# Kernel optimization log

Measured on AMD Instinct MI355X. Metric: run time of the kernel, lower is better.

## Reference

```python
import jax, jax.numpy as jnp
import numpy as np

N_SEG = 128      # number of ragged segments (boundaries has N_SEG+1 entries)
SEG_LEN = 128    # tokens per segment (regular boundaries)
D_IN = 1024      # input_size
H = 512          # hidden per direction; output_size = 2*H = 1024


def _run_dir(xs, W_ih, W_hh, b):
    """xs: [L, B, D] -> hidden states [L, B, H] for one direction.
    torch LSTM gate order: i, f, g, o."""
    xp = jnp.einsum('lbd,gd->lbg', xs, W_ih) + b  # precompute input projections [L,B,4H]
    B = xs.shape[1]
    Hh = W_hh.shape[1]

    def step(carry, gx):
        h, c = carry
        g = gx + h @ W_hh.T
        i, f, gg, o = jnp.split(g, 4, axis=-1)
        c = jax.nn.sigmoid(f) * c + jax.nn.sigmoid(i) * jnp.tanh(gg)
        h = jax.nn.sigmoid(o) * jnp.tanh(c)
        return (h, c), h

    z = jnp.zeros((B, Hh), xs.dtype)
    _, hs = jax.lax.scan(step, (z, z), xp)
    return hs


def _bilstm(x, W_ih_f, W_hh_f, b_f, W_ih_b, W_hh_b, b_b):
    hf = _run_dir(x, W_ih_f, W_hh_f, b_f)
    hb = _run_dir(x[::-1], W_ih_b, W_hh_b, b_b)[::-1]
    return jnp.concatenate([hf, hb], axis=-1)  # [L, B, 2H], fwd then bwd as in torch


def setup_inputs() -> dict:
    key = jax.random.key(0)
    ks = jax.random.split(key, 7)
    T = N_SEG * SEG_LEN
    s = 1.0 / np.sqrt(H)  # torch LSTM init scale
    u = lambda k, shape: jax.random.uniform(k, shape, jnp.float32, -s, s)
    return {
        'all_embs': jax.random.normal(ks[0], (T, D_IN), jnp.float32),
        'boundaries': jnp.arange(N_SEG + 1, dtype=jnp.int32) * SEG_LEN,
        'W_ih_f': u(ks[1], (4 * H, D_IN)),
        'W_hh_f': u(ks[2], (4 * H, H)),
        'b_f': u(ks[3], (4 * H,)),  # b_ih + b_hh folded together
        'W_ih_b': u(ks[4], (4 * H, D_IN)),
        'W_hh_b': u(ks[5], (4 * H, H)),
        'b_b': u(ks[6], (4 * H,)),
    }


def reference(all_embs, boundaries, W_ih_f, W_hh_f, b_f, W_ih_b, W_hh_b, b_b):
    n_seg = boundaries.shape[0] - 1
    T, D = all_embs.shape
    L = T // n_seg
    # regular boundaries: batch the per-segment LSTM calls into one scan
    x = all_embs.reshape(n_seg, L, D).transpose(1, 0, 2)  # [L, n_seg, D]
    y = _bilstm(x, W_ih_f, W_hh_f, b_f, W_ih_b, W_hh_b, b_b)  # [L, n_seg, 2H]
    out = y.transpose(1, 0, 2).reshape(T, 2 * H)
    # summarize=False: new boundaries equal old boundaries
    return (out, boundaries)
```

## Files before the change

kernel.cpp:

```cpp
#include <hip/hip_runtime.h>


typedef __attribute__((ext_vector_type(8))) short bf16x8;
typedef __attribute__((ext_vector_type(4))) float f32x4;

__device__ __forceinline__ unsigned short f2bf(float f) {
  unsigned int x = __builtin_bit_cast(unsigned int, f);
  x += 0x7fffu + ((x >> 16) & 1u);
  return (unsigned short)(x >> 16);
}
__device__ __forceinline__ float bf2f(unsigned short u) {
  unsigned int x = ((unsigned int)u) << 16;
  return __builtin_bit_cast(float, x);
}
__device__ __forceinline__ float sigm(float x) { return 1.f / (1.f + __expf(-x)); }
__device__ __forceinline__ float tanhfast(float x) {
  float e = __expf(2.f * x);
  return 1.f - 2.f / (e + 1.f);
}

__device__ __forceinline__ void gl_lds16(const void* g, void* l) {
  __builtin_amdgcn_global_load_lds((const __attribute__((address_space(1))) unsigned int*)g,
                                   (__attribute__((address_space(3))) unsigned int*)l, 16, 0, 0);
}
__device__ __forceinline__ void gl_lds16_llc(const void* g, void* l) {
  __builtin_amdgcn_global_load_lds((const __attribute__((address_space(1))) unsigned int*)g,
                                   (__attribute__((address_space(3))) unsigned int*)l, 16, 0, 17);
}

__global__ __launch_bounds__(256) void cast_x(const float* __restrict__ X,
                                              unsigned short* __restrict__ Xb) {
  const int i = blockIdx.x * 256 + threadIdx.x;
  const float4 v = ((const float4*)X)[i];
  uint2 o;
  o.x = (unsigned int)f2bf(v.x) | ((unsigned int)f2bf(v.y) << 16);
  o.y = (unsigned int)f2bf(v.z) | ((unsigned int)f2bf(v.w) << 16);
  ((uint2*)Xb)[i] = o;
}

__global__ __launch_bounds__(256) void pack_w(const float* __restrict__ Wif,
                                              const float* __restrict__ bf_,
                                              const float* __restrict__ Wib,
                                              const float* __restrict__ bb_,
                                              unsigned short* __restrict__ Wc,
                                              float* __restrict__ biasp) {
  const int pr = blockIdx.x;
  const int d = pr >> 11, r = pr & 2047;
  const float* src = (d ? Wib : Wif) + (size_t)r * 1024;
  const int t = threadIdx.x;
  const float4 v = ((const float4*)src)[t];
  uint2 o;
  o.x = (unsigned int)f2bf(v.x) | ((unsigned int)f2bf(v.y) << 16);
  o.y = (unsigned int)f2bf(v.z) | ((unsigned int)f2bf(v.w) << 16);
  ((uint2*)(Wc + (size_t)pr * 1024))[t] = o;
  if (t == 0) biasp[pr] = (d ? bb_ : bf_)[r];
}

__global__ __launch_bounds__(256) void gemm_xp(const unsigned short* __restrict__ A,
                                               const unsigned short* __restrict__ B,
                                               const float* __restrict__ bias,
                                               unsigned short* __restrict__ C) {
  __shared__ unsigned short SMEM[16384];
  unsigned short* As = SMEM;
  unsigned short* Bs = SMEM + 8192;
  const int tid = threadIdx.x;
  const int lane = tid & 63;
  const int wid = tid >> 6;
  const int wm = wid >> 1, wn = wid & 1;
  const long brow = (long)blockIdx.x * 128;
  const long bcol = (long)blockIdx.y * 128;

  f32x4 acc[4][4];
  const f32x4 z = {0.f, 0.f, 0.f, 0.f};
#pragma unroll
  for (int i = 0; i < 4; ++i)
#pragma unroll
    for (int j = 0; j < 4; ++j) acc[i][j] = z;

  int srow[4], scol[4];
#pragma unroll
  for (int j = 0; j < 4; ++j) {
    const int o = (j * 256 + tid) * 16;
    srow[j] = o >> 7;
    scol[j] = (o & 127) ^ ((srow[j] & 7) << 4);
  }

  for (int ks = 0; ks < 16; ++ks) {
    const int kb0 = ks * 128;
#pragma unroll
    for (int j = 0; j < 4; ++j) {
      const int o = (j * 256 + tid) * 16;
      gl_lds16((const char*)A + (brow + srow[j]) * 2048 + kb0 + scol[j], (char*)As + o);
      gl_lds16((const char*)B + (bcol + srow[j]) * 2048 + kb0 + scol[j], (char*)Bs + o);
    }
    __syncthreads();
    bf16x8 av[4][2], bv[4][2];
#pragma unroll
    for (int f = 0; f < 4; ++f) {
      const int ra = wm * 64 + f * 16 + (lane & 15);
      const int rb = wn * 64 + f * 16 + (lane & 15);
      const int swa = (ra & 7) << 4, swb = (rb & 7) << 4;
#pragma unroll
      for (int kk = 0; kk < 2; ++kk) {
        const int kby = kk * 64 + (lane >> 4) * 16;
        av[f][kk] = *(const bf16x8*)((const char*)As + ra * 128 + (kby ^ swa));
        bv[f][kk] = *(const bf16x8*)((const char*)Bs + rb * 128 + (kby ^ swb));
      }
    }
#pragma unroll
    for (int kk = 0; kk < 2; ++kk)
#pragma unroll
      for (int fm = 0; fm < 4; ++fm)
#pragma unroll
        for (int fn = 0; fn < 4; ++fn)
          acc[fm][fn] =
              __builtin_amdgcn_mfma_f32_16x16x32_bf16(av[fm][kk], bv[fn][kk], acc[fm][fn], 0, 0, 0);
    __syncthreads();
  }
  const int crow0 = wm * 64 + (lane >> 4) * 4;
  const int ccol0 = wn * 64 + (lane & 15);
#pragma unroll
  for (int fm = 0; fm < 4; ++fm) {
#pragma unroll
    for (int fn = 0; fn < 4; ++fn) {
      const int col = ccol0 + fn * 16;
      const float bsv = bias[bcol + col];
#pragma unroll
      for (int r = 0; r < 4; ++r)
        SMEM[(crow0 + fm * 16 + r) * 128 + col] = f2bf(acc[fm][fn][r] + bsv);
    }
  }
  __syncthreads();
#pragma unroll
  for (int j = 0; j < 8; ++j) {
    const int id = j * 256 + tid;
    const int row = id >> 4;
    const int c = id & 15;
    *(float4*)(C + (brow + row) * 4096 + bcol + c * 8) = *(const float4*)(SMEM + row * 128 + c * 8);
  }
}

__global__ __launch_bounds__(256, 1) void lstm_persist(
    const unsigned short* __restrict__ XPb, const float* __restrict__ Whf,
    const float* __restrict__ Whb, unsigned short* __restrict__ hb0,
    unsigned short* __restrict__ hb1, float* __restrict__ out,
    unsigned int* __restrict__ ctr) {
  __shared__ unsigned short A_s[8192];
  __shared__ unsigned short Hrep[16][32];

  const int tid = threadIdx.x;
  const int bid = blockIdx.x;
  const int ut = bid >> 4;
  const int grp = bid & 15;
  const int dir = grp >> 3;
  const int cs = grp & 7;
  const int lane = tid & 63;
  const int w = tid >> 6;
  const int p = lane & 15;
  const int kq8 = lane >> 4;
  const int hi = p >> 3;
  const int u_l = w * 8 + (p & 7);
  const int u_g = ut * 32 + u_l;
  unsigned int* const myctr = ctr + grp * 32;

  bf16x8 wreg[2][16];
  {
    const float* Wh = dir ? Whb : Whf;
#pragma unroll
    for (int f = 0; f < 2; ++f) {
      const int g = f * 2 + hi;
      const float* wrow = Wh + (size_t)(g * 512 + u_g) * 512 + kq8 * 8;
#pragma unroll
      for (int kk = 0; kk < 16; ++kk) {
        const float4 v0 = *(const float4*)(wrow + kk * 32);
        const float4 v1 = *(const float4*)(wrow + kk * 32 + 4);
        bf16x8 t;
        t[0] = (short)f2bf(v0.x); t[1] = (short)f2bf(v0.y);
        t[2] = (short)f2bf(v0.z); t[3] = (short)f2bf(v0.w);
        t[4] = (short)f2bf(v1.x); t[5] = (short)f2bf(v1.y);
        t[6] = (short)f2bf(v1.z); t[7] = (short)f2bf(v1.w);
        wreg[f][kk] = t;
      }
    }
  }

  float c_reg[2] = {0.f, 0.f};
  const size_t tileoff = (size_t)grp * 16384;
  const int cl0 = kq8 * 4 + 2 * hi;

  unsigned short xpr[2][4];
  {
    const int tcol0 = dir ? 127 : 0;
#pragma unroll
    for (int j = 0; j < 2; ++j) {
      const int seg = cs * 16 + cl0 + j;
      const size_t tok = (size_t)seg * 128 + tcol0;
      const unsigned short* xp = XPb + tok * 4096 + dir * 2048 + u_g;
#pragma unroll
      for (int g = 0; g < 4; ++g) xpr[j][g] = xp[g * 512];
    }
  }

  float phv[2];
  size_t pofs[2] = {0, 0};

  for (int tau = 0; tau < 128; ++tau) {
    const unsigned short* hc = (tau & 1) ? hb1 : hb0;
    unsigned short* hn = (tau & 1) ? hb0 : hb1;
    const int tcol = dir ? (127 - tau) : tau;

    {
      const char* srcb = (const char*)hc + tileoff;
      char* dstb = (char*)A_s;
#pragma unroll
      for (int j = 0; j < 4; ++j) {
        const int o = (j * 256 + tid) * 16;
        gl_lds16_llc(srcb + o, dstb + o);
      }
    }
    if (tau > 0) {
      out[pofs[0]] = phv[0];
      out[pofs[1]] = phv[1];
    }
    __syncthreads();

    unsigned short xprN[2][4];
    if (tau < 127) {
      const int tcolN = dir ? (126 - tau) : (tau + 1);
#pragma unroll
      for (int j = 0; j < 2; ++j) {
        const int seg = cs * 16 + cl0 + j;
        const size_t tok = (size_t)seg * 128 + tcolN;
        const unsigned short* xp = XPb + tok * 4096 + dir * 2048 + u_g;
#pragma unroll
        for (int g = 0; g < 4; ++g) xprN[j][g] = xp[g * 512];
      }
    }

    f32x4 accp[2][2];
    const f32x4 z = {0.f, 0.f, 0.f, 0.f};
    accp[0][0] = z; accp[0][1] = z; accp[1][0] = z; accp[1][1] = z;
    {
      const char* abase = (const char*)A_s + p * 1024;
      const int asw = (p & 7) << 4;
#pragma unroll
      for (int kk = 0; kk < 16; ++kk) {
        const int kb = kk * 64 + kq8 * 16;
        const bf16x8 af = *(const bf16x8*)(abase + (kb ^ asw));
        accp[0][kk & 1] =
            __builtin_amdgcn_mfma_f32_16x16x32_bf16(af, wreg[0][kk], accp[0][kk & 1], 0, 0, 0);
        accp[1][kk & 1] =
            __builtin_amdgcn_mfma_f32_16x16x32_bf16(af, wreg[1][kk], accp[1][kk & 1], 0, 0, 0);
      }
    }
    f32x4 acc0, acc1;
#pragma unroll
    for (int r = 0; r < 4; ++r) {
      acc0[r] = accp[0][0][r] + accp[0][1][r];
      acc1[r] = accp[1][0][r] + accp[1][1][r];
    }

    float hvr[2];
    {
      const float s0 = hi ? acc0[0] : acc0[2];
      const float s1 = hi ? acc0[1] : acc0[3];
      const float s2 = hi ? acc1[0] : acc1[2];
      const float s3 = hi ? acc1[1] : acc1[3];
      const float e0 = __shfl_xor(s0, 8);
      const float e1 = __shfl_xor(s1, 8);
      const float e2 = __shfl_xor(s2, 8);
      const float e3 = __shfl_xor(s3, 8);
      const float a0 = hi ? acc0[2] : acc0[0];
      const float a1 = hi ? acc0[3] : acc0[1];
      const float b0 = hi ? acc1[2] : acc1[0];
      const float b1 = hi ? acc1[3] : acc1[1];
      const float gi[2] = {hi ? e0 : a0, hi ? e1 : a1};
      const float gf[2] = {hi ? a0 : e0, hi ? a1 : e1};
      const float gg[2] = {hi ? e2 : b0, hi ? e3 : b1};
      const float go[2] = {hi ? b0 : e2, hi ? b1 : e3};
#pragma unroll
      for (int j = 0; j < 2; ++j) {
        const int cl = cl0 + j;
        const float pi = gi[j] + bf2f(xpr[j][0]);
        const float pf = gf[j] + bf2f(xpr[j][1]);
        const float pg = gg[j] + bf2f(xpr[j][2]);
        const float po = go[j] + bf2f(xpr[j][3]);
        float cv = sigm(pf) * c_reg[j] + sigm(pi) * tanhfast(pg);
        c_reg[j] = cv;
        hvr[j] = sigm(po) * tanhfast(cv);
        Hrep[cl][u_l] = f2bf(hvr[j]);
        const int seg = cs * 16 + cl;
        const size_t tok = (size_t)seg * 128 + tcol;
        pofs[j] = tok * 1024 + dir * 512 + u_g;
        phv[j] = hvr[j];
      }
    }
#pragma unroll
    for (int j = 0; j < 2; ++j)
#pragma unroll
      for (int g = 0; g < 4; ++g) xpr[j][g] = xprN[j][g];

    __syncthreads();

    if (tid < 128) {
      const int cl = tid >> 3, q = tid & 7;
      const unsigned long long v = *(const unsigned long long*)&Hrep[cl][q * 4];
      char* dst = (char*)hn + tileoff + cl * 1024 + ((ut * 64 + q * 8) ^ ((cl & 7) << 4));
      __hip_atomic_store((unsigned long long*)dst, v, __ATOMIC_RELAXED,
                         __HIP_MEMORY_SCOPE_AGENT);
    }

    __syncthreads();
    if (tid == 0) {
      const unsigned old =
          __hip_atomic_fetch_add(myctr, 1u, __ATOMIC_RELAXED, __HIP_MEMORY_SCOPE_AGENT);
      const unsigned tgt = (unsigned)(tau + 1) * 16u;
      if (old + 1u != tgt) {
        while (__hip_atomic_load(myctr, __ATOMIC_RELAXED, __HIP_MEMORY_SCOPE_AGENT) < tgt)
          __builtin_amdgcn_s_sleep(1);
      }
    }
    __syncthreads();
  }
  out[pofs[0]] = phv[0];
  out[pofs[1]] = phv[1];
}

__global__ void wr_bounds(const int* __restrict__ b, float* __restrict__ o) {
  const int i = threadIdx.x;
  if (i < 129) o[i] = (float)b[i];
}

extern "C" void kernel_launch(void* const* d_in, const int* in_sizes, int n_in,
                              void* d_out, int out_size, void* d_ws, size_t ws_size,
                              hipStream_t stream) {
  const float* X = (const float*)d_in[0];
  const int* bnd = (const int*)d_in[1];
  const float* Wif = (const float*)d_in[2];
  const float* Whf = (const float*)d_in[3];
  const float* bf_ = (const float*)d_in[4];
  const float* Wib = (const float*)d_in[5];
  const float* Whb = (const float*)d_in[6];
  const float* bb_ = (const float*)d_in[7];
  float* out = (float*)d_out;

  wr_bounds<<<1, 256, 0, stream>>>(bnd, out + 16777216);

  char* ws = (char*)d_ws;
  const size_t NEED = 176703488ULL;
  if (ws_size < NEED) return;

  unsigned short* XPb = (unsigned short*)(ws + 0);
  unsigned short* Xb = (unsigned short*)(ws + 134217728);
  unsigned short* Wc = (unsigned short*)(ws + 167772160);
  float* biasp = (float*)(ws + 176160768);
  unsigned short* hb0 = (unsigned short*)(ws + 176177152);
  unsigned short* hb1 = (unsigned short*)(ws + 176439296);
  unsigned int* ctrp = (unsigned int*)(ws + 176701440);

  cast_x<<<16384, 256, 0, stream>>>(X, Xb);
  pack_w<<<4096, 256, 0, stream>>>(Wif, bf_, Wib, bb_, Wc, biasp);
  dim3 gg(128, 32);
  gemm_xp<<<gg, 256, 0, stream>>>(Xb, Wc, biasp, XPb);

  hipMemsetAsync(hb0, 0, 262144, stream);
  hipMemsetAsync(ctrp, 0, 2048, stream);

  {
    const unsigned short* xpb = XPb;
    const float* whf = Whf;
    const float* whb = Whb;
    unsigned short* h0 = hb0;
    unsigned short* h1 = hb1;
    float* op = out;
    unsigned int* cp = ctrp;
    void* args[] = {&xpb, &whf, &whb, &h0, &h1, &op, &cp};
    hipError_t e = hipLaunchCooperativeKernel((const void*)lstm_persist, dim3(256), dim3(256),
                                              args, 0, stream);
    if (e != hipSuccess) {
      lstm_persist<<<256, 256, 0, stream>>>(XPb, Whf, Whb, hb0, hb1, out, ctrp);
    }
  }
}
```

Measured before the change: 502.2 us.

## Enlarge input-projection GEMM tile to 256x256 with double-buffered LDS prefetch

Result: faster. 488.3 us (median of 2 runs) (-2.8%).

```diff
diff --git a/kernel.cpp b/kernel.cpp
--- a/kernel.cpp
+++ b/kernel.cpp
@@ -56,87 +56,119 @@
   if (t == 0) biasp[pr] = (d ? bb_ : bf_)[r];
 }
 
-__global__ __launch_bounds__(256) void gemm_xp(const unsigned short* __restrict__ A,
+__global__ __launch_bounds__(512) void gemm_xp(const unsigned short* __restrict__ A,
                                                const unsigned short* __restrict__ B,
                                                const float* __restrict__ bias,
                                                unsigned short* __restrict__ C) {
-  __shared__ unsigned short SMEM[16384];
-  unsigned short* As = SMEM;
-  unsigned short* Bs = SMEM + 8192;
+  __shared__ unsigned short SMEM[65536];
   const int tid = threadIdx.x;
   const int lane = tid & 63;
   const int wid = tid >> 6;
-  const int wm = wid >> 1, wn = wid & 1;
-  const long brow = (long)blockIdx.x * 128;
-  const long bcol = (long)blockIdx.y * 128;
-
-  f32x4 acc[4][4];
+  const int wm = wid >> 2;
+  const int wn = wid & 3;
+  const long brow = (long)blockIdx.x * 256;
+  const long bcol = (long)blockIdx.y * 256;
+
+  f32x4 acc[8][4];
   const f32x4 z = {0.f, 0.f, 0.f, 0.f};
 #pragma unroll
-  for (int i = 0; i < 4; ++i)
-#pragma unroll
-    for (int j = 0; j < 4; ++j) acc[i][j] = z;
-
-  int srow[4], scol[4];
-#pragma unroll
-  for (int j = 0; j < 4; ++j) {
-    const int o = (j * 256 + tid) * 16;
+  for (int m = 0; m < 8; ++m)
+#pragma unroll
+    for (int n = 0; n < 4; ++n) acc[m][n] = z;
+
+  int srow[2], scol[2];
+#pragma unroll
+  for (int j = 0; j < 2; ++j) {
+    const int o = (j * 512 + tid) * 16;
     srow[j] = o >> 7;
     scol[j] = (o & 127) ^ ((srow[j] & 7) << 4);
   }
 
-  for (int ks = 0; ks < 16; ++ks) {
-    const int kb0 = ks * 128;
-#pragma unroll
-    for (int j = 0; j < 4; ++j) {
-      const int o = (j * 256 + tid) * 16;
-      gl_lds16((const char*)A + (brow + srow[j]) * 2048 + kb0 + scol[j], (char*)As + o);
-      gl_lds16((const char*)B + (bcol + srow[j]) * 2048 + kb0 + scol[j], (char*)Bs + o);
+#define STAGE_HALF(t, h, buf)                                                          \
+  do {                                                                                 \
+    const char* aA_ = (const char*)A + (brow + (h)*128) * 2048 + (t)*128;              \
+    const char* aB_ = (const char*)B + (bcol + (h)*128) * 2048 + (t)*128;              \
+    char* dA_ = (char*)(SMEM + ((buf)*2 + (h)) * 8192);                                \
+    char* dB_ = (char*)(SMEM + 32768 + ((buf)*2 + (h)) * 8192);                        \
+    _Pragma("unroll") for (int j_ = 0; j_ < 2; ++j_) {                                 \
+      const int o_ = (j_ * 512 + tid) * 16;                                            \
+      gl_lds16(aA_ + (long)srow[j_] * 2048 + scol[j_], dA_ + o_);                      \
+      gl_lds16(aB_ + (long)srow[j_] * 2048 + scol[j_], dB_ + o_);                      \
+    }                                                                                  \
+  } while (0)
+
+  STAGE_HALF(0, 0, 0);
+  STAGE_HALF(0, 1, 0);
+  __syncthreads();
+
+  const int p15 = lane & 15;
+  const int kq = lane >> 4;
+
+  for (int t = 0; t < 16; ++t) {
+    const int cur = t & 1, nxt = cur ^ 1;
+    const bool doStage = (t + 1 < 16);
+    const unsigned short* Acur = SMEM + (cur * 2 + wm) * 8192;
+    const unsigned short* Bcur = SMEM + 32768 + (cur * 2 + (wn >> 1)) * 8192;
+#pragma unroll
+    for (int p = 0; p < 4; ++p) {
+      if (p < 2 && doStage) STAGE_HALF(t + 1, p, nxt);
+      bf16x8 af[2][2], bf[4][2];
+#pragma unroll
+      for (int mm = 0; mm < 2; ++mm) {
+        const int ar = (2 * p + mm) * 16 + p15;
+        const char* abase = (const char*)Acur + ar * 128;
+        const int asw = (ar & 7) << 4;
+#pragma unroll
+        for (int kk = 0; kk < 2; ++kk)
+          af[mm][kk] = *(const bf16x8*)(abase + ((kk * 64 + kq * 16) ^ asw));
+      }
+#pragma unroll
+      for (int n = 0; n < 4; ++n) {
+        const int br = (wn & 1) * 64 + n * 16 + p15;
+        const char* bbase = (const char*)Bcur + br * 128;
+        const int bsw = (br & 7) << 4;
+#pragma unroll
+        for (int kk = 0; kk < 2; ++kk)
+          bf[n][kk] = *(const bf16x8*)(bbase + ((kk * 64 + kq * 16) ^ bsw));
+      }
+      __builtin_amdgcn_s_barrier();
+      __builtin_amdgcn_s_setprio(1);
+#pragma unroll
+      for (int kk = 0; kk < 2; ++kk)
+#pragma unroll
+        for (int mm = 0; mm < 2; ++mm)
+#pragma unroll
+          for (int n = 0; n < 4; ++n)
+            acc[2 * p + mm][n] = __builtin_amdgcn_mfma_f32_16x16x32_bf16(
+                af[mm][kk], bf[n][kk], acc[2 * p + mm][n], 0, 0, 0);
+      __builtin_amdgcn_s_setprio(0);
+      __builtin_amdgcn_s_barrier();
     }
     __syncthreads();
-    bf16x8 av[4][2], bv[4][2];
-#pragma unroll
-    for (int f = 0; f < 4; ++f) {
-      const int ra = wm * 64 + f * 16 + (lane & 15);
-      const int rb = wn * 64 + f * 16 + (lane & 15);
-      const int swa = (ra & 7) << 4, swb = (rb & 7) << 4;
-#pragma unroll
-      for (int kk = 0; kk < 2; ++kk) {
-        const int kby = kk * 64 + (lane >> 4) * 16;
-        av[f][kk] = *(const bf16x8*)((const char*)As + ra * 128 + (kby ^ swa));
-        bv[f][kk] = *(const bf16x8*)((const char*)Bs + rb * 128 + (kby ^ swb));
-      }
-    }
-#pragma unroll
-    for (int kk = 0; kk < 2; ++kk)
-#pragma unroll
-      for (int fm = 0; fm < 4; ++fm)
-#pragma unroll
-        for (int fn = 0; fn < 4; ++fn)
-          acc[fm][fn] =
-              __builtin_amdgcn_mfma_f32_16x16x32_bf16(av[fm][kk], bv[fn][kk], acc[fm][fn], 0, 0, 0);
-    __syncthreads();
-  }
-  const int crow0 = wm * 64 + (lane >> 4) * 4;
-  const int ccol0 = wn * 64 + (lane & 15);
-#pragma unroll
-  for (int fm = 0; fm < 4; ++fm) {
-#pragma unroll
-    for (int fn = 0; fn < 4; ++fn) {
-      const int col = ccol0 + fn * 16;
+  }
+#undef STAGE_HALF
+
+  const int crow0 = wm * 128 + kq * 4;
+  const int ccol0 = wn * 64 + p15;
+#pragma unroll
+  for (int m = 0; m < 8; ++m) {
+#pragma unroll
+    for (int n = 0; n < 4; ++n) {
+      const int col = ccol0 + n * 16;
       const float bsv = bias[bcol + col];
 #pragma unroll
       for (int r = 0; r < 4; ++r)
-        SMEM[(crow0 + fm * 16 + r) * 128 + col] = f2bf(acc[fm][fn][r] + bsv);
+        SMEM[(crow0 + m * 16 + r) * 256 + col] = f2bf(acc[m][n][r] + bsv);
     }
   }
   __syncthreads();
 #pragma unroll
-  for (int j = 0; j < 8; ++j) {
-    const int id = j * 256 + tid;
-    const int row = id >> 4;
-    const int c = id & 15;
-    *(float4*)(C + (brow + row) * 4096 + bcol + c * 8) = *(const float4*)(SMEM + row * 128 + c * 8);
+  for (int i = 0; i < 16; ++i) {
+    const int id = i * 512 + tid;
+    const int row = id >> 5;
+    const int c = id & 31;
+    *(float4*)(C + (brow + row) * 4096 + bcol + c * 8) =
+        *(const float4*)(SMEM + row * 256 + c * 8);
   }
 }
 
@@ -360,8 +392,8 @@
 
   cast_x<<<16384, 256, 0, stream>>>(X, Xb);
   pack_w<<<4096, 256, 0, stream>>>(Wif, bf_, Wib, bb_, Wc, biasp);
-  dim3 gg(128, 32);
-  gemm_xp<<<gg, 256, 0, stream>>>(Xb, Wc, biasp, XPb);
+  dim3 gg(64, 16);
+  gemm_xp<<<gg, 512, 0, stream>>>(Xb, Wc, biasp, XPb);
 
   hipMemsetAsync(hb0, 0, 262144, stream);
   hipMemsetAsync(ctrp, 0, 2048, stream);
```
